# Optimization experiments

Hardware: AMD Instinct MI355X
Metric: run time of the kernel (lower is better)

The kernel has to match this reference:

```python
import jax, jax.numpy as jnp
import numpy as np

B, TE, TD, D, U = 8, 256, 256, 256, 256


def setup_inputs() -> dict:
    key = jax.random.key(0)
    k1, k2, k3, k4, k5 = jax.random.split(key, 5)
    glorot = lambda k, shape: jax.random.uniform(
        k, shape, jnp.float32,
        -np.sqrt(6.0 / (shape[0] + shape[1])), np.sqrt(6.0 / (shape[0] + shape[1])))
    return {
        "en_seq": jax.random.normal(k1, (B, TE, D), jnp.float32),
        "de_seq": jax.random.normal(k2, (B, TD, D), jnp.float32),
        "w_en": glorot(k3, (D, U)),
        "w_de": glorot(k4, (D, U)),
        "nu": glorot(k5, (U, 1)),
    }


def reference(en_seq, de_seq, w_en, w_de, nu):
    # Additive co-attention scores.
    ae = jnp.einsum('bte,eu->btu', en_seq, w_en)          # (B, Te, U)
    ad = jnp.einsum('bsd,du->bsu', de_seq, w_de)          # (B, Td, U)
    # co_m[b, td, te, u] = ae[b, te, u] + ad[b, td, u]  (matches K.repeat / repeat_elements layout)
    co = jnp.tanh(ad[:, :, None, :] + ae[:, None, :, :])  # (B, Td, Te, U)
    mu = jnp.einsum('bstu,ul->bst', co, nu)               # (B, Td, Te)
    alphas = jax.nn.softmax(mu, axis=-1)                  # softmax over en time
    max_mu = jnp.max(mu, axis=-1)                         # (B, Td)
    max_alphas = jax.nn.softmax(max_mu, axis=-1)          # softmax over de time
    h_hat = jnp.sum(de_seq * max_alphas[..., None], axis=1)  # (B, Dd)
    sum_en = jnp.einsum('bst,bte->bse', alphas, en_seq)      # (B, Td, De)
    output = jnp.concatenate(
        [de_seq, sum_en, de_seq * sum_en, de_seq * h_hat[:, None, :]], axis=-1)
    return output  # (B, Td, 4*D)
```

## Files before the change

kernel.cpp:

```cpp
#include <hip/hip_runtime.h>

#define B_   8
#define TE_  256
#define TD_  256
#define D_   256
#define U_   256

#define EET_OFF   0
#define ED_OFF    524288
#define ALPHA_OFF 1048576
#define MAXMU_OFF 1572864
#define HH_OFF    1574912

__device__ __forceinline__ float fexp2(float x) {
#if __has_builtin(__builtin_amdgcn_exp2f)
  return __builtin_amdgcn_exp2f(x);
#else
  return exp2f(x);
#endif
}
__device__ __forceinline__ float frcp(float x) {
#if __has_builtin(__builtin_amdgcn_rcpf)
  return __builtin_amdgcn_rcpf(x);
#else
  return 1.0f / x;
#endif
}

#define LOG2E_F 1.4426950408889634f
#define TWO_LOG2E_F 2.8853900817779268f

__global__ __launch_bounds__(256) void coatt_k1_proj(
    const float* __restrict__ en, const float* __restrict__ de,
    const float* __restrict__ w_en, const float* __restrict__ w_de,
    float* __restrict__ ws) {
  const int which = blockIdx.z;
  const float* __restrict__ A = which ? de : en;
  const float* __restrict__ W = which ? w_de : w_en;
  const int rowBase = blockIdx.y * 64;
  const int colBase = blockIdx.x * 64;
  __shared__ float As[2][32][68];
  __shared__ float Bs[2][32][68];
  const int tid = threadIdx.x;
  const int tx = tid & 15, ty = tid >> 4;

  const int aRow0 = tid >> 3, aC4 = tid & 7;
  const int bK0 = tid >> 4, bC4 = tid & 15;
  float4 aR[2], bR[2];

#pragma unroll
  for (int kk = 0; kk < 2; ++kk) {
    aR[kk] = *(const float4*)&A[(rowBase + aRow0 + 32 * kk) * D_ + aC4 * 4];
    bR[kk] = *(const float4*)&W[(bK0 + 16 * kk) * U_ + colBase + bC4 * 4];
  }
#pragma unroll
  for (int kk = 0; kk < 2; ++kk) {
    float v[4]; *(float4*)v = aR[kk];
#pragma unroll
    for (int j = 0; j < 4; ++j) As[0][aC4 * 4 + j][aRow0 + 32 * kk] = v[j];
    *(float4*)&Bs[0][bK0 + 16 * kk][bC4 * 4] = bR[kk];
  }
  __syncthreads();

  float acc[4][4] = {};
#define K1_COMPUTE(BUF)                                            \
  _Pragma("unroll")                                                \
  for (int k = 0; k < 32; ++k) {                                   \
    float av[4], bv[4];                                            \
    *(float4*)av = *(const float4*)&As[BUF][k][ty * 4];            \
    *(float4*)bv = *(const float4*)&Bs[BUF][k][tx * 4];            \
    _Pragma("unroll")                                              \
    for (int i = 0; i < 4; ++i)                                    \
      _Pragma("unroll")                                            \
      for (int j = 0; j < 4; ++j)                                  \
        acc[i][j] = fmaf(av[i], bv[j], acc[i][j]);                 \
  }

  for (int kc = 0; kc < 7; ++kc) {
    const int k0 = (kc + 1) * 32;
#pragma unroll
    for (int kk = 0; kk < 2; ++kk) {
      aR[kk] = *(const float4*)&A[(rowBase + aRow0 + 32 * kk) * D_ + k0 + aC4 * 4];
      bR[kk] = *(const float4*)&W[(k0 + bK0 + 16 * kk) * U_ + colBase + bC4 * 4];
    }
    const int cur = kc & 1, nxt = cur ^ 1;
    K1_COMPUTE(cur)
#pragma unroll
    for (int kk = 0; kk < 2; ++kk) {
      float v[4]; *(float4*)v = aR[kk];
#pragma unroll
      for (int j = 0; j < 4; ++j) As[nxt][aC4 * 4 + j][aRow0 + 32 * kk] = v[j];
      *(float4*)&Bs[nxt][bK0 + 16 * kk][bC4 * 4] = bR[kk];
    }
    __syncthreads();
  }
  K1_COMPUTE(1)
  __syncthreads();

  if (which) {
    float* __restrict__ out = ws + ED_OFF;
#pragma unroll
    for (int i = 0; i < 4; ++i) {
      float4 o;
      o.x = fexp2(acc[i][0] * TWO_LOG2E_F);
      o.y = fexp2(acc[i][1] * TWO_LOG2E_F);
      o.z = fexp2(acc[i][2] * TWO_LOG2E_F);
      o.w = fexp2(acc[i][3] * TWO_LOG2E_F);
      *(float4*)&out[(rowBase + ty * 4 + i) * U_ + colBase + tx * 4] = o;
    }
  } else {
    float* Cs = &As[0][0][0];
#pragma unroll
    for (int i = 0; i < 4; ++i)
#pragma unroll
      for (int j = 0; j < 4; ++j)
        Cs[(tx * 4 + j) * 68 + ty * 4 + i] = fexp2(acc[i][j] * TWO_LOG2E_F);
    __syncthreads();
    float* __restrict__ out = ws + EET_OFF;
    const int b = rowBase >> 8, t0 = rowBase & 255;
#pragma unroll
    for (int kk = 0; kk < 4; ++kk) {
      const int q = tid + 256 * kk;
      const int uc = q >> 4, tq = q & 15;
      const float4 v = *(const float4*)&Cs[uc * 68 + tq * 4];
      *(float4*)&out[(size_t)(b * U_ + colBase + uc) * TE_ + t0 + tq * 4] = v;
    }
  }
}

__global__ __launch_bounds__(256) void coatt_k2_mu(
    const float* __restrict__ nu, float* __restrict__ ws) {
  const float* __restrict__ EeT = ws + EET_OFF;
  const float* __restrict__ Ed = ws + ED_OFF;
  float* __restrict__ alphas = ws + ALPHA_OFF;
  float* __restrict__ maxmu = ws + MAXMU_OFF;
  const int b = blockIdx.y;
  const int sBase = blockIdx.x * 4;
  const int tid = threadIdx.x;
  const int w = tid >> 6, lane = tid & 63;
  const float* __restrict__ Ee_b = EeT + (size_t)b * U_ * TE_ + tid;
  const float* __restrict__ Ed_b = Ed + (size_t)(b * TD_ + sBase) * U_;

  float acc0 = 0.f, acc1 = 0.f, acc2 = 0.f, acc3 = 0.f;
#pragma unroll 4
  for (int u4 = 0; u4 < 64; ++u4) {
    const float4 nv = *(const float4*)&nu[u4 * 4];
    const float4 e0 = *(const float4*)&Ed_b[0 * U_ + u4 * 4];
    const float4 e1 = *(const float4*)&Ed_b[1 * U_ + u4 * 4];
    const float4 e2 = *(const float4*)&Ed_b[2 * U_ + u4 * 4];
    const float4 e3 = *(const float4*)&Ed_b[3 * U_ + u4 * 4];
    float ee[4];
#pragma unroll
    for (int j = 0; j < 4; ++j) ee[j] = Ee_b[(u4 * 4 + j) * TE_];
    const float* nvp = (const float*)&nv;
    const float* p0 = (const float*)&e0;
    const float* p1 = (const float*)&e1;
    const float* p2 = (const float*)&e2;
    const float* p3 = (const float*)&e3;
#pragma unroll
    for (int j = 0; j < 4; ++j) {
      acc0 = fmaf(nvp[j], frcp(fmaf(p0[j], ee[j], 1.0f)), acc0);
      acc1 = fmaf(nvp[j], frcp(fmaf(p1[j], ee[j], 1.0f)), acc1);
      acc2 = fmaf(nvp[j], frcp(fmaf(p2[j], ee[j], 1.0f)), acc2);
      acc3 = fmaf(nvp[j], frcp(fmaf(p3[j], ee[j], 1.0f)), acc3);
    }
  }
  float v[4] = {-2.f * acc0, -2.f * acc1, -2.f * acc2, -2.f * acc3};
  __shared__ float part[4][4];
  float m[4];
#pragma unroll
  for (int s = 0; s < 4; ++s) {
    m[s] = v[s];
#pragma unroll
    for (int off = 32; off > 0; off >>= 1) m[s] = fmaxf(m[s], __shfl_xor(m[s], off));
    if (lane == 0) part[s][w] = m[s];
  }
  __syncthreads();
#pragma unroll
  for (int s = 0; s < 4; ++s)
    m[s] = fmaxf(fmaxf(part[s][0], part[s][1]), fmaxf(part[s][2], part[s][3]));
  __syncthreads();
  float e[4], sm[4];
#pragma unroll
  for (int s = 0; s < 4; ++s) {
    e[s] = fexp2((v[s] - m[s]) * LOG2E_F);
    sm[s] = e[s];
#pragma unroll
    for (int off = 32; off > 0; off >>= 1) sm[s] += __shfl_xor(sm[s], off);
    if (lane == 0) part[s][w] = sm[s];
  }
  __syncthreads();
  float* __restrict__ al = alphas + (size_t)(b * TD_ + sBase) * TE_;
#pragma unroll
  for (int s = 0; s < 4; ++s) {
    const float tot = (part[s][0] + part[s][1]) + (part[s][2] + part[s][3]);
    al[s * TE_ + tid] = e[s] * frcp(tot);
  }
  if (tid == 0) {
#pragma unroll
    for (int s = 0; s < 4; ++s) maxmu[b * TD_ + sBase + s] = m[s];
  }
}

__global__ __launch_bounds__(256) void coatt_k3_hhat(
    const float* __restrict__ de, float* __restrict__ ws) {
  const float* __restrict__ maxmu = ws + MAXMU_OFF;
  float* __restrict__ hhat = ws + HH_OFF;
  const int b = blockIdx.y;
  const int dBase = blockIdx.x * 32;
  const int tid = threadIdx.x;
  const int w = tid >> 6, lane = tid & 63;
  __shared__ float red[8];
  __shared__ float malpha[256];
  __shared__ float acc_red[256];
  const float v = maxmu[b * TD_ + tid];
  float m = v;
#pragma unroll
  for (int off = 32; off > 0; off >>= 1) m = fmaxf(m, __shfl_xor(m, off));
  if (lane == 0) red[w] = m;
  __syncthreads();
  m = fmaxf(fmaxf(red[0], red[1]), fmaxf(red[2], red[3]));
  const float e = fexp2((v - m) * LOG2E_F);
  float sm = e;
#pragma unroll
  for (int off = 32; off > 0; off >>= 1) sm += __shfl_xor(sm, off);
  if (lane == 0) red[4 + w] = sm;
  __syncthreads();
  sm = (red[4] + red[5]) + (red[6] + red[7]);
  malpha[tid] = e * frcp(sm);
  __syncthreads();
  const int dl = tid & 31, sg = tid >> 5;
  float acc = 0.f;
  for (int s = sg * 32; s < sg * 32 + 32; ++s)
    acc = fmaf(de[(b * TD_ + s) * D_ + dBase + dl], malpha[s], acc);
  acc_red[tid] = acc;
  __syncthreads();
  if (tid < 32) {
    float t = acc_red[tid];
#pragma unroll
    for (int g = 1; g < 8; ++g) t += acc_red[g * 32 + tid];
    hhat[b * D_ + dBase + tid] = t;
  }
}

__global__ __launch_bounds__(256) void coatt_k4_out(
    const float* __restrict__ en, const float* __restrict__ de,
    const float* __restrict__ ws, float* __restrict__ out) {
  const float* __restrict__ alphas = ws + ALPHA_OFF;
  const float* __restrict__ hhat = ws + HH_OFF;
  const int b = blockIdx.y;
  const int sBase = blockIdx.x * 4;
  const int d = threadIdx.x;
  const float* __restrict__ al = alphas + (size_t)(b * TD_ + sBase) * TE_;
  const float* __restrict__ en_b = en + (size_t)b * TE_ * D_ + d;

  float acc0 = 0.f, acc1 = 0.f, acc2 = 0.f, acc3 = 0.f;
#pragma unroll 4
  for (int t4 = 0; t4 < 64; ++t4) {
    const float4 a0 = *(const float4*)&al[0 * TE_ + t4 * 4];
    const float4 a1 = *(const float4*)&al[1 * TE_ + t4 * 4];
    const float4 a2 = *(const float4*)&al[2 * TE_ + t4 * 4];
    const float4 a3 = *(const float4*)&al[3 * TE_ + t4 * 4];
    float env[4];
#pragma unroll
    for (int j = 0; j < 4; ++j) env[j] = en_b[(t4 * 4 + j) * D_];
    const float* q0 = (const float*)&a0;
    const float* q1 = (const float*)&a1;
    const float* q2 = (const float*)&a2;
    const float* q3 = (const float*)&a3;
#pragma unroll
    for (int j = 0; j < 4; ++j) {
      acc0 = fmaf(q0[j], env[j], acc0);
      acc1 = fmaf(q1[j], env[j], acc1);
      acc2 = fmaf(q2[j], env[j], acc2);
      acc3 = fmaf(q3[j], env[j], acc3);
    }
  }
  const float hh = hhat[b * D_ + d];
  const float se[4] = {acc0, acc1, acc2, acc3};
#pragma unroll
  for (int s = 0; s < 4; ++s) {
    const float dd = de[(size_t)(b * TD_ + sBase + s) * D_ + d];
    float* o = out + (size_t)(b * TD_ + sBase + s) * (4 * D_);
    o[d] = dd;
    o[D_ + d] = se[s];
    o[2 * D_ + d] = dd * se[s];
    o[3 * D_ + d] = dd * hh;
  }
}

extern "C" void kernel_launch(void* const* d_in, const int* in_sizes, int n_in,
                              void* d_out, int out_size, void* d_ws, size_t ws_size,
                              hipStream_t stream) {
  (void)in_sizes; (void)n_in; (void)out_size; (void)ws_size;
  const float* en   = (const float*)d_in[0];
  const float* de   = (const float*)d_in[1];
  const float* w_en = (const float*)d_in[2];
  const float* w_de = (const float*)d_in[3];
  const float* nu   = (const float*)d_in[4];
  float* out = (float*)d_out;
  float* ws  = (float*)d_ws;

  coatt_k1_proj<<<dim3(4, 32, 2), 256, 0, stream>>>(en, de, w_en, w_de, ws);
  coatt_k2_mu<<<dim3(64, 8), 256, 0, stream>>>(nu, ws);
  coatt_k3_hhat<<<dim3(8, 8), 256, 0, stream>>>(de, ws);
  coatt_k4_out<<<dim3(64, 8), 256, 0, stream>>>(en, de, ws, out);
}
```

Before: 121.9 us.

## Replace shared-memory tiled projection GEMM with direct per-thread column kernel

The projection kernel drops the LDS double-buffered 64x64 tiled GEMM. Each thread now owns one output column u and accumulates 16 rows, reading W coalesced from global memory and the A rows as wave-uniform broadcast loads. This removes the LDS staging, barriers and the transpose pass through shared memory. In exchange it relies on cache for reuse and loses the register blocking that reused each loaded value across several outputs, so arithmetic intensity per load is lower. The transposed EeT store now writes float4s with a stride of TE_ between threads.

After: 173.9 us. 1.43x slower.

```diff
diff --git a/kernel.cpp b/kernel.cpp
--- a/kernel.cpp
+++ b/kernel.cpp
@@ -34,96 +34,46 @@
     const float* __restrict__ en, const float* __restrict__ de,
     const float* __restrict__ w_en, const float* __restrict__ w_de,
     float* __restrict__ ws) {
-  const int which = blockIdx.z;
+  const int bi = blockIdx.x;
+  const int which = bi >> 7;
   const float* __restrict__ A = which ? de : en;
   const float* __restrict__ W = which ? w_de : w_en;
-  const int rowBase = blockIdx.y * 64;
-  const int colBase = blockIdx.x * 64;
-  __shared__ float As[2][32][68];
-  __shared__ float Bs[2][32][68];
-  const int tid = threadIdx.x;
-  const int tx = tid & 15, ty = tid >> 4;
-
-  const int aRow0 = tid >> 3, aC4 = tid & 7;
-  const int bK0 = tid >> 4, bC4 = tid & 15;
-  float4 aR[2], bR[2];
-
-#pragma unroll
-  for (int kk = 0; kk < 2; ++kk) {
-    aR[kk] = *(const float4*)&A[(rowBase + aRow0 + 32 * kk) * D_ + aC4 * 4];
-    bR[kk] = *(const float4*)&W[(bK0 + 16 * kk) * U_ + colBase + bC4 * 4];
-  }
-#pragma unroll
-  for (int kk = 0; kk < 2; ++kk) {
-    float v[4]; *(float4*)v = aR[kk];
-#pragma unroll
-    for (int j = 0; j < 4; ++j) As[0][aC4 * 4 + j][aRow0 + 32 * kk] = v[j];
-    *(float4*)&Bs[0][bK0 + 16 * kk][bC4 * 4] = bR[kk];
-  }
-  __syncthreads();
-
-  float acc[4][4] = {};
-#define K1_COMPUTE(BUF)                                            \
-  _Pragma("unroll")                                                \
-  for (int k = 0; k < 32; ++k) {                                   \
-    float av[4], bv[4];                                            \
-    *(float4*)av = *(const float4*)&As[BUF][k][ty * 4];            \
-    *(float4*)bv = *(const float4*)&Bs[BUF][k][tx * 4];            \
-    _Pragma("unroll")                                              \
-    for (int i = 0; i < 4; ++i)                                    \
-      _Pragma("unroll")                                            \
-      for (int j = 0; j < 4; ++j)                                  \
-        acc[i][j] = fmaf(av[i], bv[j], acc[i][j]);                 \
-  }
-
-  for (int kc = 0; kc < 7; ++kc) {
-    const int k0 = (kc + 1) * 32;
-#pragma unroll
-    for (int kk = 0; kk < 2; ++kk) {
-      aR[kk] = *(const float4*)&A[(rowBase + aRow0 + 32 * kk) * D_ + k0 + aC4 * 4];
-      bR[kk] = *(const float4*)&W[(k0 + bK0 + 16 * kk) * U_ + colBase + bC4 * 4];
-    }
-    const int cur = kc & 1, nxt = cur ^ 1;
-    K1_COMPUTE(cur)
-#pragma unroll
-    for (int kk = 0; kk < 2; ++kk) {
-      float v[4]; *(float4*)v = aR[kk];
-#pragma unroll
-      for (int j = 0; j < 4; ++j) As[nxt][aC4 * 4 + j][aRow0 + 32 * kk] = v[j];
-      *(float4*)&Bs[nxt][bK0 + 16 * kk][bC4 * 4] = bR[kk];
-    }
-    __syncthreads();
-  }
-  K1_COMPUTE(1)
-  __syncthreads();
+  const int rowBase = (bi & 127) * 16;
+  const int u = threadIdx.x;
+
+  float acc[16] = {};
+#pragma unroll 4
+  for (int k4 = 0; k4 < 64; ++k4) {
+    float wv[4];
+#pragma unroll
+    for (int j = 0; j < 4; ++j) wv[j] = W[(k4 * 4 + j) * U_ + u];
+#pragma unroll
+    for (int i = 0; i < 16; ++i) {
+      const float4 a4 = *(const float4*)&A[(rowBase + i) * D_ + k4 * 4];
+      acc[i] = fmaf(a4.x, wv[0], acc[i]);
+      acc[i] = fmaf(a4.y, wv[1], acc[i]);
+      acc[i] = fmaf(a4.z, wv[2], acc[i]);
+      acc[i] = fmaf(a4.w, wv[3], acc[i]);
+    }
+  }
 
   if (which) {
     float* __restrict__ out = ws + ED_OFF;
 #pragma unroll
-    for (int i = 0; i < 4; ++i) {
-      float4 o;
-      o.x = fexp2(acc[i][0] * TWO_LOG2E_F);
-      o.y = fexp2(acc[i][1] * TWO_LOG2E_F);
-      o.z = fexp2(acc[i][2] * TWO_LOG2E_F);
-      o.w = fexp2(acc[i][3] * TWO_LOG2E_F);
-      *(float4*)&out[(rowBase + ty * 4 + i) * U_ + colBase + tx * 4] = o;
-    }
+    for (int i = 0; i < 16; ++i)
+      out[(rowBase + i) * U_ + u] = fexp2(acc[i] * TWO_LOG2E_F);
   } else {
-    float* Cs = &As[0][0][0];
-#pragma unroll
-    for (int i = 0; i < 4; ++i)
-#pragma unroll
-      for (int j = 0; j < 4; ++j)
-        Cs[(tx * 4 + j) * 68 + ty * 4 + i] = fexp2(acc[i][j] * TWO_LOG2E_F);
-    __syncthreads();
     float* __restrict__ out = ws + EET_OFF;
     const int b = rowBase >> 8, t0 = rowBase & 255;
-#pragma unroll
-    for (int kk = 0; kk < 4; ++kk) {
-      const int q = tid + 256 * kk;
-      const int uc = q >> 4, tq = q & 15;
-      const float4 v = *(const float4*)&Cs[uc * 68 + tq * 4];
-      *(float4*)&out[(size_t)(b * U_ + colBase + uc) * TE_ + t0 + tq * 4] = v;
+    float* __restrict__ p = out + (size_t)(b * U_ + u) * TE_ + t0;
+#pragma unroll
+    for (int q = 0; q < 4; ++q) {
+      float4 o;
+      o.x = fexp2(acc[q * 4 + 0] * TWO_LOG2E_F);
+      o.y = fexp2(acc[q * 4 + 1] * TWO_LOG2E_F);
+      o.z = fexp2(acc[q * 4 + 2] * TWO_LOG2E_F);
+      o.w = fexp2(acc[q * 4 + 3] * TWO_LOG2E_F);
+      *(float4*)&p[q * 4] = o;
     }
   }
 }
@@ -301,7 +251,7 @@
   float* out = (float*)d_out;
   float* ws  = (float*)d_ws;
 
-  coatt_k1_proj<<<dim3(4, 32, 2), 256, 0, stream>>>(en, de, w_en, w_de, ws);
+  coatt_k1_proj<<<dim3(256), 256, 0, stream>>>(en, de, w_en, w_de, ws);
   coatt_k2_mu<<<dim3(64, 8), 256, 0, stream>>>(nu, ws);
   coatt_k3_hhat<<<dim3(8, 8), 256, 0, stream>>>(de, ws);
   coatt_k4_out<<<dim3(64, 8), 256, 0, stream>>>(en, de, ws, out);
```
